# Kernel tuning notes

Hardware: AMD Instinct MI355X
Metric: run time of the kernel (lower is better)

Reference implementation:

```python
import jax, jax.numpy as jnp
import numpy as np

SPD = 24


def setup_inputs() -> dict:
    key = jax.random.key(0)
    k1, k2 = jax.random.split(key)
    x = jax.random.normal(k1, (128, 1024, 768), dtype=jnp.float32)
    # stand-in for orthogonally-initialized projection weight [spd_dim, in_dim]
    W = jax.random.normal(k2, (SPD, 768), dtype=jnp.float32) / np.float32(np.sqrt(768.0))
    return {"x": x, "W": W}


def reference(x, W):
    # projection: nn.Linear(bias=False) -> x @ W.T, [B, T, spd]
    p = jnp.einsum('btd,kd->btk', x, W)
    p = p - jnp.mean(p, axis=1, keepdims=True)
    n = p.shape[1]
    # covariance [B, spd, spd]
    cov = jnp.einsum('btk,btl->bkl', p, p) / (n - 1 + 1e-6)
    trace = jnp.trace(cov, axis1=-2, axis2=-1)[:, None, None]
    cov = cov / (trace + 1e-6)
    cov = (cov + jnp.swapaxes(cov, -1, -2)) / 2
    cov = cov + 1e-4 * jnp.eye(SPD, dtype=cov.dtype)
    eig_vals, eig_vecs = jnp.linalg.eigh(cov)
    log_vals = jnp.log(jnp.clip(eig_vals, 1e-6))
    # V diag(log_vals) V^T
    log_cov = jnp.einsum('bik,bk,bjk->bij', eig_vecs, log_vals, eig_vecs)
    iu, ju = jnp.triu_indices(SPD)
    return log_cov[:, iu, ju]  # [B, spd*(spd+1)/2]
```

## Files before the change

### kernel.cpp

```cpp
#include <hip/hip_runtime.h>
#include <math.h>


#define AS1 __attribute__((address_space(1)))
#define AS3 __attribute__((address_space(3)))

#define B_      128
#define T_      1024
#define D_      768
#define K_      24
#define ROWS    256
#define BPB     4
#define DCHUNK  32
#define CHW     8192
#define PSTRIDE 28
#define NACC    600
#define NPAIR   300
#define SWEEPS  8

__global__ __launch_bounds__(256, 2) void socpool_proj(
    const float* __restrict__ x, const float* __restrict__ W,
    float* __restrict__ partial) {
  __shared__ float smem[2 * CHW];
  const int tid  = threadIdx.x;
  const int b    = blockIdx.x >> 2;
  const int rb   = blockIdx.x & 3;
  const int wv   = tid >> 6;
  const int lane = tid & 63;
  const float* xbase = x + ((size_t)b * T_ + rb * ROWS) * D_;

  float acc[K_];
#pragma unroll
  for (int k = 0; k < K_; ++k) acc[k] = 0.f;

  auto issue = [&](int dc, int bufsel) {
    float* buf = smem + bufsel * CHW;
#pragma unroll
    for (int it = 0; it < 8; ++it) {
      const int fl  = it * 256 + wv * 64 + lane;
      const int row = fl >> 3;
      const int qlg = (fl & 7) ^ (row & 7);
      const float* g = xbase + (size_t)row * D_ + (dc + (qlg << 2));
      float* l = buf + (size_t)(it * 256 + wv * 64) * 4;
      __builtin_amdgcn_global_load_lds((const AS1 void*)g, (AS3 void*)l,
                                       16, 0, 0);
    }
  };

  issue(0, 0);
  __syncthreads();
  for (int c = 0; c < D_ / DCHUNK; ++c) {
    if (c + 1 < D_ / DCHUNK) issue((c + 1) * DCHUNK, (c + 1) & 1);
    const float* buf = smem + (c & 1) * CHW;
    const int dc = c * DCHUNK;
#pragma unroll
    for (int qd = 0; qd < 8; ++qd) {
      float4 xv = *(const float4*)(&buf[tid * 32 + ((qd ^ (tid & 7)) << 2)]);
      const float* wp = W + dc + (qd << 2);
#pragma unroll
      for (int k = 0; k < K_; ++k) {
        const float* wr = wp + (size_t)k * D_;
        acc[k] = fmaf(xv.x, wr[0], acc[k]);
        acc[k] = fmaf(xv.y, wr[1], acc[k]);
        acc[k] = fmaf(xv.z, wr[2], acc[k]);
        acc[k] = fmaf(xv.w, wr[3], acc[k]);
      }
    }
    __syncthreads();
  }

  float* P = smem;
#pragma unroll
  for (int q = 0; q < 6; ++q)
    *(float4*)(&P[tid * PSTRIDE + 4 * q]) =
        make_float4(acc[4*q], acc[4*q+1], acc[4*q+2], acc[4*q+3]);
  __syncthreads();
  float* outp = partial + (size_t)blockIdx.x * NACC;
  if (tid < 144) {
    const int k = tid / 6;
    const int q = (tid % 6) * 4;
    float a0=0.f,a1=0.f,a2=0.f,a3=0.f,b0=0.f,b1=0.f,b2=0.f,b3=0.f;
    for (int t = 0; t < ROWS; t += 2) {
      float  pk0 = P[t * PSTRIDE + k];
      float4 pq0 = *(const float4*)(&P[t * PSTRIDE + q]);
      float  pk1 = P[(t + 1) * PSTRIDE + k];
      float4 pq1 = *(const float4*)(&P[(t + 1) * PSTRIDE + q]);
      a0 = fmaf(pk0, pq0.x, a0); a1 = fmaf(pk0, pq0.y, a1);
      a2 = fmaf(pk0, pq0.z, a2); a3 = fmaf(pk0, pq0.w, a3);
      b0 = fmaf(pk1, pq1.x, b0); b1 = fmaf(pk1, pq1.y, b1);
      b2 = fmaf(pk1, pq1.z, b2); b3 = fmaf(pk1, pq1.w, b3);
    }
    outp[k * K_ + q + 0] = a0 + b0;
    outp[k * K_ + q + 1] = a1 + b1;
    outp[k * K_ + q + 2] = a2 + b2;
    outp[k * K_ + q + 3] = a3 + b3;
  } else if (tid < 168) {
    const int k = tid - 144;
    float s0 = 0.f, s1 = 0.f;
    for (int t = 0; t < ROWS; t += 2) {
      s0 += P[t * PSTRIDE + k];
      s1 += P[(t + 1) * PSTRIDE + k];
    }
    outp[576 + k] = s0 + s1;
  }
}

__global__ __launch_bounds__(64, 1) void socpool_eig(
    const float* __restrict__ partial, float* __restrict__ out) {
  __shared__ float Amat[K_ * 25];
  __shared__ float Qs[K_ * 25];
  __shared__ float lv[K_];
  __shared__ float raw[NACC];
  __shared__ float Xc[K_ * PSTRIDE];
  const int tid = threadIdx.x;
  const int b = blockIdx.x;

#pragma unroll
  for (int i = 0; i < 10; ++i) {
    int e = tid + (i << 6);
    if (e < NACC) {
      float v = 0.f;
#pragma unroll
      for (int jj = 0; jj < BPB; ++jj)
        v += partial[(size_t)(b * BPB + jj) * NACC + e];
      raw[e] = v;
    }
  }
  __syncthreads();

  const float inv_n   = 1.f / 1024.f;
  const float inv_nm1 = 1.f / (1023.f + 1e-6f);
  float cv[9];
#pragma unroll
  for (int i = 0; i < 9; ++i) {
    int e = tid + (i << 6);
    int k = e / K_, l = e % K_;
    cv[i] = (raw[e] - raw[576 + k] * raw[576 + l] * inv_n) * inv_nm1;
    Amat[k * 25 + l] = cv[i];
  }
  __syncthreads();
  float tr = 0.f;
#pragma unroll
  for (int k = 0; k < K_; ++k) tr += Amat[k * 25 + k];
  float sym[9];
#pragma unroll
  for (int i = 0; i < 9; ++i) {
    int e = tid + (i << 6);
    int k = e / K_, l = e % K_;
    sym[i] = cv[i] + Amat[l * 25 + k];
  }
  __syncthreads();
  const float sc = 0.5f / (tr + 1e-6f);
#pragma unroll
  for (int i = 0; i < 9; ++i) {
    int e = tid + (i << 6);
    int k = e / K_, l = e % K_;
    Amat[k * 25 + l] = sym[i] * sc + ((k == l) ? 1e-4f : 0.f);
  }
  __syncthreads();

  const int j = tid;
  float4 Gv[6];
#pragma unroll
  for (int q = 0; q < 6; ++q) {
    Gv[q].x = (j < K_) ? Amat[j * 25 + 4*q + 0] : 0.f;
    Gv[q].y = (j < K_) ? Amat[j * 25 + 4*q + 1] : 0.f;
    Gv[q].z = (j < K_) ? Amat[j * 25 + 4*q + 2] : 0.f;
    Gv[q].w = (j < K_) ? Amat[j * 25 + 4*q + 3] : 0.f;
  }

  for (int sweep = 0; sweep < SWEEPS; ++sweep) {
    for (int rr = 0; rr < 23; ++rr) {
      int partner;
      if (j == 23) {
        partner = (12 * rr) % 23;
      } else if (j < 23) {
        partner = rr - j;
        if (partner < 0) partner += 23;
        if (partner == j) partner = 23;
      } else {
        partner = j;
      }
      if (j < K_) {
#pragma unroll
        for (int q = 0; q < 6; ++q)
          *(float4*)(&Xc[j * PSTRIDE + (q << 2)]) = Gv[q];
      }
      __syncthreads();
      const int pcol = (partner < K_) ? partner : 0;
      float4 O[6];
#pragma unroll
      for (int q = 0; q < 6; ++q)
        O[q] = *(const float4*)(&Xc[pcol * PSTRIDE + (q << 2)]);
      float a0=0.f,a1=0.f,a2=0.f,a3=0.f;
      float b0=0.f,b1=0.f,b2=0.f,b3=0.f;
      float c0=0.f,c1=0.f,c2=0.f,c3=0.f;
#pragma unroll
      for (int q = 0; q < 6; ++q) {
        a0 = fmaf(Gv[q].x, Gv[q].x, a0); a1 = fmaf(Gv[q].y, Gv[q].y, a1);
        a2 = fmaf(Gv[q].z, Gv[q].z, a2); a3 = fmaf(Gv[q].w, Gv[q].w, a3);
        b0 = fmaf(O[q].x, O[q].x, b0);   b1 = fmaf(O[q].y, O[q].y, b1);
        b2 = fmaf(O[q].z, O[q].z, b2);   b3 = fmaf(O[q].w, O[q].w, b3);
        c0 = fmaf(Gv[q].x, O[q].x, c0);  c1 = fmaf(Gv[q].y, O[q].y, c1);
        c2 = fmaf(Gv[q].z, O[q].z, c2);  c3 = fmaf(Gv[q].w, O[q].w, c3);
      }
      float nn  = (a0 + a1) + (a2 + a3);
      float nno = (b0 + b1) + (b2 + b3);
      float gpq = (c0 + c1) + (c2 + c3);
      const bool low = (j < partner);
      float app = low ? nn : nno;
      float aqq = low ? nno : nn;
      float cc = 1.f, ss = 0.f;
      if (j != partner && fabsf(gpq) > 1e-30f) {
        float tau = (aqq - app) / (2.f * gpq);
        float t = 1.f / (fabsf(tau) + sqrtf(1.f + tau * tau));
        if (tau < 0.f) t = -t;
        cc = 1.f / sqrtf(1.f + t * t);
        ss = t * cc;
      }
      float sg = low ? -ss : ss;
#pragma unroll
      for (int q = 0; q < 6; ++q) {
        Gv[q].x = fmaf(sg, O[q].x, cc * Gv[q].x);
        Gv[q].y = fmaf(sg, O[q].y, cc * Gv[q].y);
        Gv[q].z = fmaf(sg, O[q].z, cc * Gv[q].z);
        Gv[q].w = fmaf(sg, O[q].w, cc * Gv[q].w);
      }
      __syncthreads();
    }
  }

  if (j < K_) {
    float n0=0.f,n1=0.f,n2=0.f,n3=0.f;
#pragma unroll
    for (int q = 0; q < 6; ++q) {
      n0 = fmaf(Gv[q].x, Gv[q].x, n0); n1 = fmaf(Gv[q].y, Gv[q].y, n1);
      n2 = fmaf(Gv[q].z, Gv[q].z, n2); n3 = fmaf(Gv[q].w, Gv[q].w, n3);
    }
    float lam = sqrtf((n0 + n1) + (n2 + n3));
    lv[j] = logf(fmaxf(lam, 1e-6f));
    float inv = 1.f / fmaxf(lam, 1e-20f);
#pragma unroll
    for (int q = 0; q < 6; ++q) {
      Qs[(4*q + 0) * 25 + j] = Gv[q].x * inv;
      Qs[(4*q + 1) * 25 + j] = Gv[q].y * inv;
      Qs[(4*q + 2) * 25 + j] = Gv[q].z * inv;
      Qs[(4*q + 3) * 25 + j] = Gv[q].w * inv;
    }
  }
  __syncthreads();

  for (int e = tid; e < NPAIR; e += 64) {
    int i = 0, base = 0;
    while (i < K_ - 1 && base + (K_ - i) <= e) { base += K_ - i; ++i; }
    int jj = i + (e - base);
    float sum = 0.f;
#pragma unroll
    for (int k = 0; k < K_; ++k)
      sum = fmaf(Qs[i * 25 + k] * lv[k], Qs[jj * 25 + k], sum);
    out[(size_t)b * NPAIR + e] = sum;
  }
}

extern "C" void kernel_launch(void* const* d_in, const int* in_sizes, int n_in,
                              void* d_out, int out_size, void* d_ws, size_t ws_size,
                              hipStream_t stream) {
  const float* x = (const float*)d_in[0];
  const float* W = (const float*)d_in[1];
  float* partial = (float*)d_ws;
  float* out = (float*)d_out;
  hipLaunchKernelGGL(socpool_proj, dim3(B_ * BPB), dim3(256), 0, stream,
                     x, W, partial);
  hipLaunchKernelGGL(socpool_eig, dim3(B_), dim3(64), 0, stream,
                     partial, out);
}
```

Baseline: 873.3 us.

## Split projection over waves by D-slice with LDS atomic row reduction

Reorganizes the projection so each wavefront handles a 24-column slice of a 96-column chunk for 64 rows at a time, rather than each thread owning a full row across all of D. Partial row projections from the four waves are combined into the shared P buffer with LDS atomicAdd after each group of eight chunks. The apparent goal is to cut redundant W loads per thread, since each wave now reads a distinct W slice, and to change the chunking of the async global-to-LDS loads. The cost is extra LDS atomics, a larger shared-memory footprint that may lower occupancy, and more complex swizzled address math.

```diff
diff --git a/kernel.cpp b/kernel.cpp
--- a/kernel.cpp
+++ b/kernel.cpp
@@ -11,8 +11,13 @@
 #define K_      24
 #define ROWS    256
 #define BPB     4
-#define DCHUNK  32
-#define CHW     8192
+#define GROWS   64
+#define NG      4
+#define DCOLS   96
+#define NCC     8
+#define NCH     32
+#define CHW     6144
+#define GRPB    196608
 #define PSTRIDE 28
 #define NACC    600
 #define NPAIR   300
@@ -21,42 +26,59 @@
 __global__ __launch_bounds__(256, 2) void socpool_proj(
     const float* __restrict__ x, const float* __restrict__ W,
     float* __restrict__ partial) {
-  __shared__ float smem[2 * CHW];
+  __shared__ float smem[2 * CHW + ROWS * PSTRIDE];
+  float* P = smem + 2 * CHW;
   const int tid  = threadIdx.x;
   const int b    = blockIdx.x >> 2;
   const int rb   = blockIdx.x & 3;
   const int wv   = tid >> 6;
-  const int lane = tid & 63;
-  const float* xbase = x + ((size_t)b * T_ + rb * ROWS) * D_;
+  const int l    = tid & 63;
+  const char* xslab = (const char*)(x + ((size_t)b * T_ + rb * ROWS) * D_);
+
+  for (int i = tid; i < ROWS * PSTRIDE; i += 256) P[i] = 0.f;
 
   float acc[K_];
 #pragma unroll
   for (int k = 0; k < K_; ++k) acc[k] = 0.f;
 
-  auto issue = [&](int dc, int bufsel) {
-    float* buf = smem + bufsel * CHW;
-#pragma unroll
-    for (int it = 0; it < 8; ++it) {
-      const int fl  = it * 256 + wv * 64 + lane;
-      const int row = fl >> 3;
-      const int qlg = (fl & 7) ^ (row & 7);
-      const float* g = xbase + (size_t)row * D_ + (dc + (qlg << 2));
-      float* l = buf + (size_t)(it * 256 + wv * 64) * 4;
-      __builtin_amdgcn_global_load_lds((const AS1 void*)g, (AS3 void*)l,
-                                       16, 0, 0);
-    }
+  int goff[6];
+#pragma unroll
+  for (int i = 0; i < 6; ++i) {
+    const int f    = (wv * 6 + i) * 1024 + l * 16;
+    const int n    = f >> 7;
+    const int row  = (n * 171) >> 9;
+    const int srel = (f - row * 384) >> 4;
+    const int Q    = (srel & ~7) | ((srel & 7) ^ (row & 7));
+    goff[i] = row * 3072 + (Q << 4);
+  }
+  int xoff[6];
+#pragma unroll
+  for (int q = 0; q < 6; ++q) {
+    const int Q = wv * 6 + q;
+    const int s = (Q & ~7) | ((Q & 7) ^ (l & 7));
+    xoff[q] = l * 96 + (s << 2);
+  }
+
+  auto issue = [&](int c, int bufsel) {
+    const int g = c >> 3, cc = c & 7;
+    const char* gbase = xslab + (size_t)g * GRPB + cc * 384;
+    float* lb = smem + bufsel * CHW + wv * 1536;
+#pragma unroll
+    for (int i = 0; i < 6; ++i)
+      __builtin_amdgcn_global_load_lds((const AS1 void*)(gbase + goff[i]),
+                                       (AS3 void*)(lb + i * 256), 16, 0, 0);
   };
 
   issue(0, 0);
   __syncthreads();
-  for (int c = 0; c < D_ / DCHUNK; ++c) {
-    if (c + 1 < D_ / DCHUNK) issue((c + 1) * DCHUNK, (c + 1) & 1);
+  for (int c = 0; c < NCH; ++c) {
+    if (c + 1 < NCH) issue(c + 1, (c + 1) & 1);
     const float* buf = smem + (c & 1) * CHW;
-    const int dc = c * DCHUNK;
-#pragma unroll
-    for (int qd = 0; qd < 8; ++qd) {
-      float4 xv = *(const float4*)(&buf[tid * 32 + ((qd ^ (tid & 7)) << 2)]);
-      const float* wp = W + dc + (qd << 2);
+    const float* wb = W + (c & 7) * DCOLS + wv * 24;
+#pragma unroll
+    for (int q = 0; q < 6; ++q) {
+      float4 xv = *(const float4*)(&buf[xoff[q]]);
+      const float* wp = wb + (q << 2);
 #pragma unroll
       for (int k = 0; k < K_; ++k) {
         const float* wr = wp + (size_t)k * D_;
@@ -66,15 +88,17 @@
         acc[k] = fmaf(xv.w, wr[3], acc[k]);
       }
     }
+    if ((c & 7) == 7) {
+      const int rbase = ((c >> 3) * GROWS + l) * PSTRIDE;
+#pragma unroll
+      for (int k = 0; k < K_; ++k) {
+        atomicAdd(&P[rbase + k], acc[k]);
+        acc[k] = 0.f;
+      }
+    }
     __syncthreads();
   }
 
-  float* P = smem;
-#pragma unroll
-  for (int q = 0; q < 6; ++q)
-    *(float4*)(&P[tid * PSTRIDE + 4 * q]) =
-        make_float4(acc[4*q], acc[4*q+1], acc[4*q+2], acc[4*q+3]);
-  __syncthreads();
   float* outp = partial + (size_t)blockIdx.x * NACC;
   if (tid < 144) {
     const int k = tid / 6;
```

Measured after the change: 1.112 ms. 1.27x slower.

## Rework projection kernel: W in LDS, lane-split D with wave reductions, register covariance

Applied to the files above, without the earlier changes.

The projection kernel now stages all of W in LDS and has each wave own whole rows. Lanes split the 768-wide dot product, and each row-by-K result is reduced with DPP and shuffle all-reduces. x is loaded straight from global into registers with double buffering, replacing the async global-to-LDS path. Covariance partials are built in registers via shuffles and then merged through LDS atomics, removing the separate per-block outer-product pass over shared memory. The catch is 24 full-wave reductions per row, each a chain of DPP steps plus two cross-lane shuffles, which may make the kernel bound on reduction latency instead of memory.

```diff
diff --git a/kernel.cpp b/kernel.cpp
--- a/kernel.cpp
+++ b/kernel.cpp
@@ -1,108 +1,136 @@
 #include <hip/hip_runtime.h>
 #include <math.h>
 
-
-#define AS1 __attribute__((address_space(1)))
-#define AS3 __attribute__((address_space(3)))
 
 #define B_      128
 #define T_      1024
 #define D_      768
 #define K_      24
-#define ROWS    256
 #define BPB     4
-#define DCHUNK  32
-#define CHW     8192
-#define PSTRIDE 28
 #define NACC    600
 #define NPAIR   300
 #define SWEEPS  8
+#define PSTRIDE 28
+
+template <int CTRL>
+__device__ __forceinline__ float dpp_add(float v) {
+  int r = __builtin_amdgcn_update_dpp(0, __float_as_int(v), CTRL, 0xF, 0xF,
+                                      false);
+  return v + __int_as_float(r);
+}
+
+__device__ __forceinline__ float allreduce64(float v) {
+  v = dpp_add<0x121>(v);
+  v = dpp_add<0x122>(v);
+  v = dpp_add<0x124>(v);
+  v = dpp_add<0x128>(v);
+  v += __shfl_xor(v, 16);
+  v += __shfl_xor(v, 32);
+  return v;
+}
 
 __global__ __launch_bounds__(256, 2) void socpool_proj(
     const float* __restrict__ x, const float* __restrict__ W,
     float* __restrict__ partial) {
-  __shared__ float smem[2 * CHW];
-  const int tid  = threadIdx.x;
-  const int b    = blockIdx.x >> 2;
-  const int rb   = blockIdx.x & 3;
-  const int wv   = tid >> 6;
-  const int lane = tid & 63;
-  const float* xbase = x + ((size_t)b * T_ + rb * ROWS) * D_;
-
-  float acc[K_];
-#pragma unroll
-  for (int k = 0; k < K_; ++k) acc[k] = 0.f;
-
-  auto issue = [&](int dc, int bufsel) {
-    float* buf = smem + bufsel * CHW;
-#pragma unroll
-    for (int it = 0; it < 8; ++it) {
-      const int fl  = it * 256 + wv * 64 + lane;
-      const int row = fl >> 3;
-      const int qlg = (fl & 7) ^ (row & 7);
-      const float* g = xbase + (size_t)row * D_ + (dc + (qlg << 2));
-      float* l = buf + (size_t)(it * 256 + wv * 64) * 4;
-      __builtin_amdgcn_global_load_lds((const AS1 void*)g, (AS3 void*)l,
-                                       16, 0, 0);
-    }
+  __shared__ __align__(16) float WL[K_ * D_];
+  __shared__ float Sbuf[NACC];
+  const int tid = threadIdx.x;
+  const int wv  = tid >> 6;
+  const int l   = tid & 63;
+
+  {
+    const float4* Wg4 = (const float4*)W;
+    float4* WL4w = (float4*)WL;
+#pragma unroll
+    for (int i = 0; i < (K_ * D_ / 4) / 256; ++i)
+      WL4w[i * 256 + tid] = Wg4[i * 256 + tid];
+  }
+  for (int e = tid; e < NACC; e += 256) Sbuf[e] = 0.f;
+
+  int ki[9], li[9];
+#pragma unroll
+  for (int i = 0; i < 9; ++i) {
+    const int e = l + (i << 6);
+    ki[i] = e / K_;
+    li[i] = e - ki[i] * K_;
+  }
+
+  float Sacc[9];
+#pragma unroll
+  for (int i = 0; i < 9; ++i) Sacc[i] = 0.f;
+  float smacc = 0.f;
+
+  const int rowbase = blockIdx.x * 256 + wv * 64;
+  const float4* x4 = (const float4*)x;
+  const float4* WL4 = (const float4*)WL;
+
+  float4 xa[4][3], xb[4][3];
+
+  auto loadg = [&](float4(&buf)[4][3], int g) {
+    const size_t base = (size_t)(rowbase + g * 4) * (D_ / 4) + l;
+#pragma unroll
+    for (int r = 0; r < 4; ++r)
+#pragma unroll
+      for (int s = 0; s < 3; ++s)
+        buf[r][s] = x4[base + r * (D_ / 4) + s * 64];
   };
 
-  issue(0, 0);
-  __syncthreads();
-  for (int c = 0; c < D_ / DCHUNK; ++c) {
-    if (c + 1 < D_ / DCHUNK) issue((c + 1) * DCHUNK, (c + 1) & 1);
-    const float* buf = smem + (c & 1) * CHW;
-    const int dc = c * DCHUNK;
-#pragma unroll
-    for (int qd = 0; qd < 8; ++qd) {
-      float4 xv = *(const float4*)(&buf[tid * 32 + ((qd ^ (tid & 7)) << 2)]);
-      const float* wp = W + dc + (qd << 2);
-#pragma unroll
-      for (int k = 0; k < K_; ++k) {
-        const float* wr = wp + (size_t)k * D_;
-        acc[k] = fmaf(xv.x, wr[0], acc[k]);
-        acc[k] = fmaf(xv.y, wr[1], acc[k]);
-        acc[k] = fmaf(xv.z, wr[2], acc[k]);
-        acc[k] = fmaf(xv.w, wr[3], acc[k]);
-      }
-    }
-    __syncthreads();
-  }
-
-  float* P = smem;
-#pragma unroll
-  for (int q = 0; q < 6; ++q)
-    *(float4*)(&P[tid * PSTRIDE + 4 * q]) =
-        make_float4(acc[4*q], acc[4*q+1], acc[4*q+2], acc[4*q+3]);
+  auto computeg = [&](const float4(&buf)[4][3]) {
+    float pk[4] = {0.f, 0.f, 0.f, 0.f};
+#pragma unroll 4
+    for (int k = 0; k < K_; ++k) {
+      const float4* wp = WL4 + k * (D_ / 4) + l;
+      const float4 w0 = wp[0];
+      const float4 w1 = wp[64];
+      const float4 w2 = wp[128];
+#pragma unroll
+      for (int r = 0; r < 4; ++r) {
+        float a;
+        a = buf[r][0].x * w0.x;
+        a = fmaf(buf[r][0].y, w0.y, a);
+        a = fmaf(buf[r][0].z, w0.z, a);
+        a = fmaf(buf[r][0].w, w0.w, a);
+        a = fmaf(buf[r][1].x, w1.x, a);
+        a = fmaf(buf[r][1].y, w1.y, a);
+        a = fmaf(buf[r][1].z, w1.z, a);
+        a = fmaf(buf[r][1].w, w1.w, a);
+        a = fmaf(buf[r][2].x, w2.x, a);
+        a = fmaf(buf[r][2].y, w2.y, a);
+        a = fmaf(buf[r][2].z, w2.z, a);
+        a = fmaf(buf[r][2].w, w2.w, a);
+        a = allreduce64(a);
+        pk[r] = (l == k) ? a : pk[r];
+      }
+    }
+#pragma unroll
+    for (int r = 0; r < 4; ++r) {
+      const float pv = pk[r];
+#pragma unroll
+      for (int i = 0; i < 9; ++i) {
+        const float va = __shfl(pv, ki[i]);
+        const float vb = __shfl(pv, li[i]);
+        Sacc[i] = fmaf(va, vb, Sacc[i]);
+      }
+      if (l < K_) smacc += pv;
+    }
+  };
+
+  __syncthreads();
+
+  loadg(xa, 0);
+  for (int g = 0; g < 16; g += 2) {
+    loadg(xb, g + 1);
+    computeg(xa);
+    if (g + 2 < 16) loadg(xa, g + 2);
+    computeg(xb);
+  }
+
+#pragma unroll
+  for (int i = 0; i < 9; ++i) atomicAdd(&Sbuf[l + (i << 6)], Sacc[i]);
+  if (l < K_) atomicAdd(&Sbuf[576 + l], smacc);
   __syncthreads();
   float* outp = partial + (size_t)blockIdx.x * NACC;
-  if (tid < 144) {
-    const int k = tid / 6;
-    const int q = (tid % 6) * 4;
-    float a0=0.f,a1=0.f,a2=0.f,a3=0.f,b0=0.f,b1=0.f,b2=0.f,b3=0.f;
-    for (int t = 0; t < ROWS; t += 2) {
-      float  pk0 = P[t * PSTRIDE + k];
-      float4 pq0 = *(const float4*)(&P[t * PSTRIDE + q]);
-      float  pk1 = P[(t + 1) * PSTRIDE + k];
-      float4 pq1 = *(const float4*)(&P[(t + 1) * PSTRIDE + q]);
-      a0 = fmaf(pk0, pq0.x, a0); a1 = fmaf(pk0, pq0.y, a1);
-      a2 = fmaf(pk0, pq0.z, a2); a3 = fmaf(pk0, pq0.w, a3);
-      b0 = fmaf(pk1, pq1.x, b0); b1 = fmaf(pk1, pq1.y, b1);
-      b2 = fmaf(pk1, pq1.z, b2); b3 = fmaf(pk1, pq1.w, b3);
-    }
-    outp[k * K_ + q + 0] = a0 + b0;
-    outp[k * K_ + q + 1] = a1 + b1;
-    outp[k * K_ + q + 2] = a2 + b2;
-    outp[k * K_ + q + 3] = a3 + b3;
-  } else if (tid < 168) {
-    const int k = tid - 144;
-    float s0 = 0.f, s1 = 0.f;
-    for (int t = 0; t < ROWS; t += 2) {
-      s0 += P[t * PSTRIDE + k];
-      s1 += P[(t + 1) * PSTRIDE + k];
-    }
-    outp[576 + k] = s0 + s1;
-  }
+  for (int e = tid; e < NACC; e += 256) outp[e] = Sbuf[e];
 }
 
 __global__ __launch_bounds__(64, 1) void socpool_eig(
@@ -269,7 +297,7 @@
   const float* W = (const float*)d_in[1];
   float* partial = (float*)d_ws;
   float* out = (float*)d_out;
-  hipLaunchKernelGGL(socpool_proj, dim3(B_ * BPB), dim3(256), 0, stream,
+  hipLaunchKernelGGL(socpool_proj, dim3(512), dim3(256), 0, stream,
                      x, W, partial);
   hipLaunchKernelGGL(socpool_eig, dim3(B_), dim3(64), 0, stream,
                      partial, out);
```

After: 742.6 us. 15.0% less time.
